# Optimization experiments

Measured on AMD Instinct MI355X. Metric: run time of the kernel, lower is better.

Reference implementation:

```python
import jax, jax.numpy as jnp
import numpy as np

D_MODEL = 1024
H = 16
D_K = D_MODEL // H
D_FF = 4096
EPS = 1e-6
NEG = -1e9


def layer_norm(x, alpha, beta):
    # Custom LN: scalar alpha/beta, unbiased std, eps added to std (not var)
    mean = jnp.mean(x, axis=-1, keepdims=True)
    std = jnp.std(x, axis=-1, ddof=1, keepdims=True)
    return alpha * (x - mean) / (std + EPS) + beta


def setup_inputs() -> dict:
    key = jax.random.key(0)
    ks = jax.random.split(key, 16)
    B, S = 4, 2048
    s = 1.0 / np.sqrt(D_MODEL)
    inp = {
        "x": jax.random.normal(ks[0], (B, S, D_MODEL), dtype=jnp.float32),
        "src_mask": jax.random.randint(ks[1], (B, 1, 1, S), 0, 2, dtype=jnp.int32),
        "wq": jax.random.normal(ks[2], (D_MODEL, D_MODEL), jnp.float32) * s,
        "bq": jnp.zeros((D_MODEL,), jnp.float32),
        "wk": jax.random.normal(ks[3], (D_MODEL, D_MODEL), jnp.float32) * s,
        "bk": jnp.zeros((D_MODEL,), jnp.float32),
        "wv": jax.random.normal(ks[4], (D_MODEL, D_MODEL), jnp.float32) * s,
        "bv": jnp.zeros((D_MODEL,), jnp.float32),
        "wo": jax.random.normal(ks[5], (D_MODEL, D_MODEL), jnp.float32) * s,
        "bo": jnp.zeros((D_MODEL,), jnp.float32),
        "w1": jax.random.normal(ks[6], (D_MODEL, D_FF), jnp.float32) * s,
        "b1": jnp.zeros((D_FF,), jnp.float32),
        "w2": jax.random.normal(ks[7], (D_FF, D_MODEL), jnp.float32) * (1.0 / np.sqrt(D_FF)),
        "b2": jnp.zeros((D_MODEL,), jnp.float32),
        "a1": jnp.ones((1,), jnp.float32),
        "be1": jnp.zeros((1,), jnp.float32),
        "a2": jnp.ones((1,), jnp.float32),
        "be2": jnp.zeros((1,), jnp.float32),
    }
    return inp


def reference(x, src_mask, wq, bq, wk, bk, wv, bv, wo, bo, w1, b1, w2, b2, a1, be1, a2, be2):
    B, S, _ = x.shape

    # --- residual 1: self-attention on pre-LN input (dropout = identity, eval) ---
    xn = layer_norm(x, a1, be1)
    q = (xn @ wq + bq).reshape(B, S, H, D_K).transpose(0, 2, 1, 3)  # [B,H,S,Dk]
    k = (xn @ wk + bk).reshape(B, S, H, D_K).transpose(0, 2, 1, 3)
    v = (xn @ wv + bv).reshape(B, S, H, D_K).transpose(0, 2, 1, 3)

    scores = jnp.einsum("bhqd,bhkd->bhqk", q, k) / jnp.sqrt(jnp.float32(D_K))
    scores = jnp.where(src_mask == 0, jnp.float32(NEG), scores)
    attn = jax.nn.softmax(scores, axis=-1)
    ctx = jnp.einsum("bhqk,bhkd->bhqd", attn, v)  # [B,H,S,Dk]
    ctx = ctx.transpose(0, 2, 1, 3).reshape(B, S, D_MODEL)
    attn_out = ctx @ wo + bo
    x = x + attn_out

    # --- residual 2: feed-forward on pre-LN input ---
    xn2 = layer_norm(x, a2, be2)
    ff = jax.nn.relu(xn2 @ w1 + b1) @ w2 + b2
    return x + ff
```

## Files before the change

kernel.cpp:

```cpp
#include <hip/hip_runtime.h>
#include <stdint.h>

typedef unsigned short u16;
typedef __attribute__((ext_vector_type(8))) short short8;
typedef __attribute__((ext_vector_type(4))) float f32x4;
typedef __attribute__((ext_vector_type(4))) u16 u16x4;
typedef __attribute__((ext_vector_type(4))) uint32_t u32x4;

#define NB 4
#define SEQ 2048
#define DM 1024
#define NH 16
#define DKh 64
#define DFF 4096
#define LOG2E 1.44269504089f

__device__ __forceinline__ u16 f2bf(float f) {
  union { float f; uint32_t u; } v; v.f = f;
  uint32_t u = v.u;
  return (u16)((u + 0x7FFFu + ((u >> 16) & 1u)) >> 16);
}

__device__ __forceinline__ uint32_t cvtpk(float lo, float hi) {
  uint32_t r;
  asm("v_cvt_pk_bf16_f32 %0, %1, %2" : "=v"(r) : "v"(lo), "v"(hi));
  return r;
}

__device__ __forceinline__ float fexp2(float x) {
  float r;
  asm("v_exp_f32 %0, %1" : "=v"(r) : "v"(x));
  return r;
}

__device__ __forceinline__ void gl16(const u16* g, u16* l) {
  __builtin_amdgcn_global_load_lds((const __attribute__((address_space(1))) void*)g,
                                   (__attribute__((address_space(3))) void*)l, 16, 0, 0);
}

__global__ __launch_bounds__(256) void transpose_bf16(const float* __restrict__ src,
                                                      u16* __restrict__ dst, int R, int C) {
  __shared__ float tile[32][33];
  int tx = threadIdx.x, ty = threadIdx.y;
  int c0 = blockIdx.x * 32, r0 = blockIdx.y * 32;
#pragma unroll
  for (int i = 0; i < 32; i += 8)
    tile[ty + i][tx] = src[(size_t)(r0 + ty + i) * C + c0 + tx];
  __syncthreads();
#pragma unroll
  for (int i = 0; i < 32; i += 8)
    dst[(size_t)(c0 + ty + i) * R + r0 + tx] = f2bf(tile[tx][ty + i]);
}

__global__ __launch_bounds__(256) void bias_cat(const float* __restrict__ bq,
                                                const float* __restrict__ bk,
                                                const float* __restrict__ bv,
                                                float* __restrict__ o) {
  int i = blockIdx.x * 256 + threadIdx.x;
  if (i < 3072) o[i] = (i < 1024) ? bq[i] : ((i < 2048) ? bk[i - 1024] : bv[i - 2048]);
}

__global__ __launch_bounds__(1024) void compact_idx(const int* __restrict__ msk,
                                                    int* __restrict__ cidx,
                                                    int* __restrict__ lArr,
                                                    int* __restrict__ lpArr,
                                                    float* __restrict__ fbbc) {
  int b = blockIdx.x;
  int t = threadIdx.x;
  int lane = t & 63, w = t >> 6;
  int i0 = t * 2, i1 = t * 2 + 1;
  int m0 = msk[b * SEQ + i0] ? 1 : 0;
  int m1 = msk[b * SEQ + i1] ? 1 : 0;
  int s = m0 + m1;
  int run = s;
#pragma unroll
  for (int d = 1; d < 64; d <<= 1) {
    int v = __shfl_up(run, d);
    if (lane >= d) run += v;
  }
  __shared__ int wtot[16];
  __shared__ int woff[17];
  if (lane == 63) wtot[w] = run;
  __syncthreads();
  if (t == 0) {
    int acc = 0;
#pragma unroll
    for (int i = 0; i < 16; ++i) { woff[i] = acc; acc += wtot[i]; }
    woff[16] = acc;
  }
  __syncthreads();
  int excl = run - s + woff[w];
  if (m0) cidx[b * SEQ + excl] = i0;
  if (m1) cidx[b * SEQ + excl + m0] = i1;
  int L = woff[16];
  int LP = (L + 63) & ~63;
  if (LP == 0) LP = 64;
  if (t == 0) { lArr[b] = L; lpArr[b] = LP; }
  for (int l = t; l < SEQ; l += 1024) {
    if (l >= L) cidx[b * SEQ + l] = 0;
    fbbc[b * SEQ + l] = (l < L) ? 0.0f : -1e9f;
  }
}

__global__ __launch_bounds__(256) void gather_vt(const u16* __restrict__ vtb,
                                                 const int* __restrict__ cidx,
                                                 const int* __restrict__ lpArr,
                                                 u16* __restrict__ vthat) {
  int d = blockIdx.x;
  int bh = blockIdx.y;
  int b = bh >> 4;
  int t = threadIdx.x;
  __shared__ u16 row[SEQ];
  const u16* src = vtb + ((size_t)bh * DKh + d) * SEQ;
  *(short8*)&row[t * 8] = *(const short8*)(src + t * 8);
  __syncthreads();
  int LP = lpArr[b];
  u16* dst = vthat + ((size_t)bh * DKh + d) * SEQ;
  const int* ib = cidx + b * SEQ;
  for (int l2 = t; l2 * 2 < LP; l2 += 256) {
    uint32_t lo = row[ib[l2 * 2]];
    uint32_t hi = row[ib[l2 * 2 + 1]];
    *(uint32_t*)&dst[l2 * 2] = lo | (hi << 16);
  }
}

__global__ __launch_bounds__(256) void ln_bf16(const float* __restrict__ x,
                                               u16* __restrict__ out,
                                               const float* __restrict__ alpha,
                                               const float* __restrict__ beta) {
  int row = blockIdx.x;
  const float4* xr = (const float4*)(x + (size_t)row * DM);
  int t = threadIdx.x;
  float4 v = xr[t];
  float s = v.x + v.y + v.z + v.w;
  float s2 = v.x * v.x + v.y * v.y + v.z * v.z + v.w * v.w;
#pragma unroll
  for (int m = 1; m < 64; m <<= 1) { s += __shfl_xor(s, m); s2 += __shfl_xor(s2, m); }
  __shared__ float red[8];
  int wid = t >> 6, lane = t & 63;
  if (lane == 0) { red[wid] = s; red[wid + 4] = s2; }
  __syncthreads();
  float S = red[0] + red[1] + red[2] + red[3];
  float S2 = red[4] + red[5] + red[6] + red[7];
  float mean = S * (1.0f / DM);
  float var = fmaxf((S2 - S * mean) * (1.0f / (DM - 1)), 0.0f);
  float inv = alpha[0] / (sqrtf(var) + 1e-6f);
  float bet = beta[0];
  u16x4 o;
  o[0] = f2bf((v.x - mean) * inv + bet);
  o[1] = f2bf((v.y - mean) * inv + bet);
  o[2] = f2bf((v.z - mean) * inv + bet);
  o[3] = f2bf((v.w - mean) * inv + bet);
  *(u16x4*)(out + (size_t)row * DM + t * 4) = o;
}

template <int MODE>
__global__ __launch_bounds__(512, 1) void gemm256(const u16* __restrict__ A,
                                                  const u16* __restrict__ WT,
                                                  const float* __restrict__ bias,
                                                  u16* __restrict__ outp,
                                                  int M, int N, int K, float qscale) {
  extern __shared__ u16 lds[];
  int tid = threadIdx.x;
  int lane = tid & 63, wid = tid >> 6;
  int lr = lane & 15, lg = lane >> 4;
  int wr = wid >> 2, wc = wid & 3;
  int nbx = N >> 8;
  int nwg = (M >> 8) * nbx;
  int lid = blockIdx.x;
  int swz = (lid & 7) * (nwg >> 3) + (lid >> 3);
  int m0 = (swz / nbx) << 8, n0 = (swz % nbx) << 8;

  int rowih = wid * 16 + (lane >> 2);
  int cchunk = lane & 3;
  int csrc = cchunk ^ ((rowih >> 1) & 3);
  size_t a_src = (size_t)(m0 + rowih) * K + csrc * 8;
  size_t b_src = (size_t)(n0 + rowih) * K + csrc * 8;
  u16* a_dst = lds + rowih * 32 + cchunk * 8;
  u16* b_dst = a_dst + 8192;

#define STAGE_A(B_, T_) do { \
    const u16* s_ = A + a_src + (size_t)(T_) * 32; \
    gl16(s_, a_dst + (B_) * 16384); \
    gl16(s_ + (size_t)128 * K, a_dst + (B_) * 16384 + 4096); \
  } while (0)
#define STAGE_B(B_, T_) do { \
    const u16* s_ = WT + b_src + (size_t)(T_) * 32; \
    gl16(s_, b_dst + (B_) * 16384); \
    gl16(s_ + (size_t)128 * K, b_dst + (B_) * 16384 + 4096); \
  } while (0)

  int rchunk = (lg ^ ((lr >> 1) & 3)) * 8;
  int offA[8], offB[4];
#pragma unroll
  for (int i = 0; i < 8; ++i) offA[i] = (wr * 128 + i * 16 + lr) * 32 + rchunk;
#pragma unroll
  for (int j = 0; j < 4; ++j) offB[j] = (wc * 64 + j * 16 + lr) * 32 + rchunk;

  f32x4 acc[8][4] = {};

  int NT = K >> 5;
  STAGE_A(0, 0); STAGE_B(0, 0);
  STAGE_A(1, 1); STAGE_B(1, 1);
  asm volatile("s_waitcnt vmcnt(4)" ::: "memory");
  __builtin_amdgcn_s_barrier();

  int buf = 0;
  for (int t = 0; t < NT; ++t) {
    const u16* la = lds + buf * 16384;
    const u16* lb = la + 8192;
    int b2 = buf - 1; if (b2 < 0) b2 += 3;
    short8 af0[4], bfr[4];
#pragma unroll
    for (int i = 0; i < 4; ++i) af0[i] = *(const short8*)&la[offA[i]];
#pragma unroll
    for (int j = 0; j < 4; ++j) bfr[j] = *(const short8*)&lb[offB[j]];
    if (t + 2 < NT) STAGE_A(b2, t + 2);
    __builtin_amdgcn_s_setprio(1);
#pragma unroll
    for (int i = 0; i < 4; ++i)
#pragma unroll
      for (int j = 0; j < 4; ++j)
        acc[i][j] = __builtin_amdgcn_mfma_f32_16x16x32_bf16(af0[i], bfr[j], acc[i][j], 0, 0, 0);
    __builtin_amdgcn_s_setprio(0);
    short8 af1[4];
#pragma unroll
    for (int i = 0; i < 4; ++i) af1[i] = *(const short8*)&la[offA[i + 4]];
    if (t + 2 < NT) STAGE_B(b2, t + 2);
    if (t < NT - 2) asm volatile("s_waitcnt vmcnt(4)" ::: "memory");
    else            asm volatile("s_waitcnt vmcnt(0)" ::: "memory");
    __builtin_amdgcn_s_setprio(1);
#pragma unroll
    for (int i = 0; i < 4; ++i)
#pragma unroll
      for (int j = 0; j < 4; ++j)
        acc[i + 4][j] = __builtin_amdgcn_mfma_f32_16x16x32_bf16(af1[i], bfr[j], acc[i + 4][j], 0, 0, 0);
    __builtin_amdgcn_s_setprio(0);
    __builtin_amdgcn_s_barrier();
    __builtin_amdgcn_sched_barrier(0);
    buf = (buf == 2) ? 0 : buf + 1;
  }
#undef STAGE_A
#undef STAGE_B

#pragma unroll
  for (int i = 0; i < 8; ++i) {
#pragma unroll
    for (int j = 0; j < 4; ++j) {
      int col = n0 + wc * 64 + j * 16 + lr;
      float bi = bias[col];
      int rbase = m0 + wr * 128 + i * 16 + lg * 4;
      if (MODE == 0) {
        int which = col >> 10, nc = col & 1023;
        int hh = nc >> 6, dd = nc & 63;
        int bb = rbase >> 11, ss = rbase & 2047;
        if (which == 2) {
          u16* vtb = outp + (size_t)2 * (8u << 20);
          u16x4 pk;
#pragma unroll
          for (int r = 0; r < 4; ++r) pk[r] = f2bf(acc[i][j][r] + bi);
          *(u16x4*)&vtb[((size_t)(bb * NH + hh) * DKh + dd) * SEQ + ss] = pk;
        } else {
          u16* dst = outp + (size_t)which * (8u << 20);
          float sc = (which == 0) ? qscale : 1.0f;
#pragma unroll
          for (int r = 0; r < 4; ++r)
            dst[((size_t)(bb * NH + hh) * SEQ + (ss + r)) * DKh + dd] = f2bf((acc[i][j][r] + bi) * sc);
        }
      } else {
#pragma unroll
        for (int r = 0; r < 4; ++r)
          outp[(size_t)(rbase + r) * N + col] = f2bf(fmaxf(acc[i][j][r] + bi, 0.0f));
      }
    }
  }
}

__global__ __launch_bounds__(512, 4) void gemm_v2(const u16* __restrict__ A,
                                                  const u16* __restrict__ WT,
                                                  const float* __restrict__ bias,
                                                  const float* __restrict__ resid,
                                                  float* __restrict__ outp,
                                                  int M, int N, int K) {
  extern __shared__ u16 lds[];
  int tid = threadIdx.x;
  int lane = tid & 63, wid = tid >> 6;
  int lr = lane & 15, lg = lane >> 4;
  int wr = wid >> 1, wc = wid & 1;
  int nbx = N >> 7;
  int nwg = (M >> 8) * nbx;
  int lid = blockIdx.x;
  int swz = (lid & 7) * (nwg >> 3) + (lid >> 3);
  int m0 = (swz / nbx) << 8, n0 = (swz % nbx) << 7;

  int sr = tid >> 2;
  int sch = tid & 3;
  int scs = sch ^ ((sr >> 1) & 3);
  size_t a_src = (size_t)(m0 + sr) * K + scs * 8;
  size_t b_src = (size_t)(n0 + sr) * K + scs * 8;
  u16* a_dst = lds + sr * 32 + sch * 8;
  u16* b_dst = lds + 8192 + sr * 32 + sch * 8;

#define STAGE(B_, T_) do { \
    gl16(A + a_src + (size_t)(T_) * 32, a_dst + (B_) * 12288); \
    gl16(A + a_src + (size_t)128 * K + (size_t)(T_) * 32, a_dst + (B_) * 12288 + 4096); \
    gl16(WT + b_src + (size_t)(T_) * 32, b_dst + (B_) * 12288); \
  } while (0)

  int rchunk = (lg ^ ((lr >> 1) & 3)) * 8;
  int offA[4], offB[4];
#pragma unroll
  for (int i = 0; i < 4; ++i) offA[i] = (wr * 64 + i * 16 + lr) * 32 + rchunk;
#pragma unroll
  for (int j = 0; j < 4; ++j) offB[j] = 8192 + (wc * 64 + j * 16 + lr) * 32 + rchunk;

  f32x4 acc[4][4] = {};

  int NT = K >> 5;
  STAGE(0, 0);
  STAGE(1, 1);
  asm volatile("s_waitcnt vmcnt(3)" ::: "memory");
  __builtin_amdgcn_s_barrier();

  int buf = 0;
  for (int t = 0; t < NT; ++t) {
    const u16* la = lds + buf * 12288;
    int b2 = buf - 1; if (b2 < 0) b2 += 3;
    short8 af[4], bfr[4];
#pragma unroll
    for (int i = 0; i < 4; ++i) af[i] = *(const short8*)&la[offA[i]];
#pragma unroll
    for (int j = 0; j < 4; ++j) bfr[j] = *(const short8*)&la[offB[j]];
    if (t + 2 < NT) STAGE(b2, t + 2);
    __builtin_amdgcn_s_setprio(1);
#pragma unroll
    for (int i = 0; i < 4; ++i)
#pragma unroll
      for (int j = 0; j < 4; ++j)
        acc[i][j] = __builtin_amdgcn_mfma_f32_16x16x32_bf16(af[i], bfr[j], acc[i][j], 0, 0, 0);
    __builtin_amdgcn_s_setprio(0);
    if (t < NT - 2) asm volatile("s_waitcnt vmcnt(3)" ::: "memory");
    else            asm volatile("s_waitcnt vmcnt(0)" ::: "memory");
    __builtin_amdgcn_s_barrier();
    __builtin_amdgcn_sched_barrier(0);
    buf = (buf == 2) ? 0 : buf + 1;
  }
#undef STAGE

#pragma unroll
  for (int i = 0; i < 4; ++i) {
#pragma unroll
    for (int j = 0; j < 4; ++j) {
      int col = n0 + wc * 64 + j * 16 + lr;
      float bi = bias[col];
      int rbase = m0 + wr * 64 + i * 16 + lg * 4;
#pragma unroll
      for (int r = 0; r < 4; ++r) {
        size_t idx = (size_t)(rbase + r) * N + col;
        outp[idx] = resid[idx] + acc[i][j][r] + bi;
      }
    }
  }
}

__global__ __launch_bounds__(256) void attn_fwd(const u16* __restrict__ q,
                                                const u16* __restrict__ k,
                                                const u16* __restrict__ vt,
                                                const int* __restrict__ cidx,
                                                const int* __restrict__ lArr,
                                                const int* __restrict__ lpArr,
                                                const float* __restrict__ fbbc,
                                                u16* __restrict__ ctx) {
  __shared__ u16 Ks[64 * 64];
  __shared__ u16 Vs[64 * 64];
  int tid = threadIdx.x;
  int wid = tid >> 6, lane = tid & 63;
  int lr = lane & 15, lg = lane >> 4;
  int bh = blockIdx.y;
  int b = bh >> 4, hh = bh & 15;
  int q0 = blockIdx.x * 128;
  const u16* qbase = q + (size_t)bh * SEQ * DKh;
  const u16* kbase = k + (size_t)bh * SEQ * DKh;
  const u16* vbase = vt + (size_t)bh * DKh * SEQ;
  const float* fbbase = fbbc + b * SEQ;
  const int* ib = cidx + b * SEQ;
  int Lb = lArr[b];
  int LP = lpArr[b];

  short8 qf[2][2];
#pragma unroll
  for (int i = 0; i < 2; ++i)
#pragma unroll
    for (int kk = 0; kk < 2; ++kk)
      qf[i][kk] = *(const short8*)(qbase + (size_t)(q0 + wid * 32 + i * 16 + lr) * DKh + kk * 32 + lg * 8);

  int sr = tid >> 3;
  int scg = (tid & 7) * 8;
  int kwix[2];
#pragma unroll
  for (int it = 0; it < 2; ++it) {
    int r = it * 32 + sr;
    kwix[it] = r * 64 + (scg ^ ((r & 7) << 3));
  }
  int jsrc = scg >> 4;
  int pos1 = (jsrc & 1) * 32 + ((scg & 15) >> 2) * 8 + (jsrc >> 1) * 4;
  int vwix[2][2];
#pragma unroll
  for (int it = 0; it < 2; ++it) {
    int r = it * 32 + sr;
    int sw = (r & 7) << 3;
    vwix[it][0] = r * 64 + (pos1 ^ sw);
    vwix[it][1] = r * 64 + ((pos1 + 8) ^ sw);
  }
  int swzc = (lr & 7) << 3;

  short8 ka[2], va[2];
  {
    int id0 = ib[sr], id1 = ib[32 + sr];
    ka[0] = *(const short8*)(kbase + (size_t)id0 * DKh + scg);
    ka[1] = *(const short8*)(kbase + (size_t)id1 * DKh + scg);
    va[0] = *(const short8*)(vbase + (size_t)sr * SEQ + scg);
    va[1] = *(const short8*)(vbase + (size_t)(32 + sr) * SEQ + scg);
  }

  f32x4 ot[2][4] = {};
  float mrow[2] = {-3e38f, -3e38f};
  float lsum[2] = {0.0f, 0.0f};

  for (int kv0 = 0; kv0 < LP; kv0 += 64) {
    __syncthreads();
#pragma unroll
    for (int it = 0; it < 2; ++it) {
      *(short8*)&Ks[kwix[it]] = ka[it];
      u16x4 vlo, vhi;
#pragma unroll
      for (int e = 0; e < 4; ++e) { vlo[e] = ((u16*)&va[it])[e]; vhi[e] = ((u16*)&va[it])[e + 4]; }
      *(u16x4*)&Vs[vwix[it][0]] = vlo;
      *(u16x4*)&Vs[vwix[it][1]] = vhi;
    }
    if (kv0 + 64 < LP) {
      int nv = kv0 + 64;
      int id0 = ib[nv + sr], id1 = ib[nv + 32 + sr];
      ka[0] = *(const short8*)(kbase + (size_t)id0 * DKh + scg);
      ka[1] = *(const short8*)(kbase + (size_t)id1 * DKh + scg);
      va[0] = *(const short8*)(vbase + (size_t)sr * SEQ + nv + scg);
      va[1] = *(const short8*)(vbase + (size_t)(32 + sr) * SEQ + nv + scg);
    }
    __syncthreads();

    f32x4 st[2][4] = {};
    __builtin_amdgcn_s_setprio(1);
#pragma unroll
    for (int kk = 0; kk < 2; ++kk) {
      short8 kf[4];
#pragma unroll
      for (int j = 0; j < 4; ++j)
        kf[j] = *(const short8*)&Ks[(j * 16 + lr) * 64 + ((kk * 32 + lg * 8) ^ swzc)];
#pragma unroll
      for (int i = 0; i < 2; ++i)
#pragma unroll
        for (int j = 0; j < 4; ++j)
          st[i][j] = __builtin_amdgcn_mfma_f32_16x16x32_bf16(kf[j], qf[i][kk], st[i][j], 0, 0, 0);
    }
    __builtin_amdgcn_s_setprio(0);

    bool tail = (kv0 + 64 > Lb);

    u32x4 pa[2][2];
#pragma unroll
    for (int i = 0; i < 2; ++i) {
      float p[4][4];
      if (tail) {
#pragma unroll
        for (int j = 0; j < 4; ++j) {
          float4 f4 = *(const float4*)(fbbase + kv0 + j * 16 + lg * 4);
          p[j][0] = st[i][j][0] + f4.x;
          p[j][1] = st[i][j][1] + f4.y;
          p[j][2] = st[i][j][2] + f4.z;
          p[j][3] = st[i][j][3] + f4.w;
        }
      } else {
#pragma unroll
        for (int j = 0; j < 4; ++j)
#pragma unroll
          for (int r = 0; r < 4; ++r) p[j][r] = st[i][j][r];
      }
      float mx = -3e38f;
#pragma unroll
      for (int j = 0; j < 4; ++j)
#pragma unroll
        for (int r = 0; r < 4; ++r) mx = fmaxf(mx, p[j][r]);
      mx = fmaxf(mx, __shfl_xor(mx, 16));
      mx = fmaxf(mx, __shfl_xor(mx, 32));
      float mnew = fmaxf(mrow[i], mx);
      if (!__all(mnew - mrow[i] <= 8.0f)) {
        float corr = fexp2(mrow[i] - mnew);
        lsum[i] *= corr;
#pragma unroll
        for (int jd = 0; jd < 4; ++jd)
#pragma unroll
          for (int r = 0; r < 4; ++r) ot[i][jd][r] *= corr;
        mrow[i] = mnew;
      }
      float ps = 0.0f;
#pragma unroll
      for (int j = 0; j < 4; ++j)
#pragma unroll
        for (int r = 0; r < 4; ++r) {
          float pv = fexp2(p[j][r] - mrow[i]);
          p[j][r] = pv;
          ps += pv;
        }
      ps += __shfl_xor(ps, 16);
      ps += __shfl_xor(ps, 32);
      lsum[i] += ps;
#pragma unroll
      for (int ks = 0; ks < 2; ++ks) {
        pa[i][ks][0] = cvtpk(p[ks][0], p[ks][1]);
        pa[i][ks][1] = cvtpk(p[ks][2], p[ks][3]);
        pa[i][ks][2] = cvtpk(p[ks + 2][0], p[ks + 2][1]);
        pa[i][ks][3] = cvtpk(p[ks + 2][2], p[ks + 2][3]);
      }
    }

    __builtin_amdgcn_s_setprio(1);
#pragma unroll
    for (int ks = 0; ks < 2; ++ks) {
      short8 vf[4];
#pragma unroll
      for (int jd = 0; jd < 4; ++jd)
        vf[jd] = *(const short8*)&Vs[(jd * 16 + lr) * 64 + ((ks * 32 + lg * 8) ^ swzc)];
#pragma unroll
      for (int i = 0; i < 2; ++i)
#pragma unroll
        for (int jd = 0; jd < 4; ++jd)
          ot[i][jd] = __builtin_amdgcn_mfma_f32_16x16x32_bf16(vf[jd], *(short8*)&pa[i][ks], ot[i][jd], 0, 0, 0);
    }
    __builtin_amdgcn_s_setprio(0);
  }

  float inv0 = 1.0f / lsum[0], inv1 = 1.0f / lsum[1];
  __syncthreads();
  u16* ep = (wid < 2) ? (Ks + wid * 2048) : (Vs + (wid - 2) * 2048);
#pragma unroll
  for (int i = 0; i < 2; ++i) {
    float inv = i ? inv1 : inv0;
#pragma unroll
    for (int jd = 0; jd < 4; ++jd) {
      uint32_t w0 = cvtpk(ot[i][jd][0] * inv, ot[i][jd][1] * inv);
      uint32_t w1 = cvtpk(ot[i][jd][2] * inv, ot[i][jd][3] * inv);
      uint32_t pk2[2] = {w0, w1};
      *(u16x4*)&ep[(i * 16 + lr) * 64 + ((jd * 16 + lg * 4) ^ swzc)] = *(u16x4*)pk2;
    }
  }
  __syncthreads();
  int q_ = lane >> 1;
  size_t orow = ((size_t)b * SEQ + q0 + wid * 32 + q_) * DM + hh * DKh;
#pragma unroll
  for (int it = 0; it < 4; ++it) {
    int dc = (lane & 1) * 32 + it * 8;
    short8 vv = *(const short8*)&ep[q_ * 64 + (dc ^ ((q_ & 7) << 3))];
    *(short8*)(ctx + orow + dc) = vv;
  }
}

extern "C" void kernel_launch(void* const* d_in, const int* in_sizes, int n_in,
                              void* d_out, int out_size, void* d_ws, size_t ws_size,
                              hipStream_t stream) {
  const float* x   = (const float*)d_in[0];
  const int*   msk = (const int*)d_in[1];
  const float* wq  = (const float*)d_in[2];
  const float* bq  = (const float*)d_in[3];
  const float* wk  = (const float*)d_in[4];
  const float* bk  = (const float*)d_in[5];
  const float* wv  = (const float*)d_in[6];
  const float* bv  = (const float*)d_in[7];
  const float* wo  = (const float*)d_in[8];
  const float* bo  = (const float*)d_in[9];
  const float* w1  = (const float*)d_in[10];
  const float* b1  = (const float*)d_in[11];
  const float* w2  = (const float*)d_in[12];
  const float* b2  = (const float*)d_in[13];
  const float* a1  = (const float*)d_in[14];
  const float* be1 = (const float*)d_in[15];
  const float* a2  = (const float*)d_in[16];
  const float* be2 = (const float*)d_in[17];
  float* out = (float*)d_out;

  u16* wqT = (u16*)d_ws;
  u16* wkT = wqT + (1u << 20);
  u16* wvT = wkT + (1u << 20);
  u16* woT = wvT + (1u << 20);
  u16* w1T = woT + (1u << 20);
  u16* w2T = w1T + (4u << 20);
  u16* xn  = w2T + (4u << 20);
  u16* qb  = xn  + (8u << 20);
  u16* kb  = qb  + (8u << 20);
  u16* vtb = kb  + (8u << 20);
  u16* ctx = vtb + (8u << 20);
  u16* hb  = qb;
  float* bcat = (float*)ctx;
  int*   cidx = (int*)(ctx + (8u << 20));
  int*   lArr = cidx + NB * SEQ;
  int*   lpArr = lArr + 16;
  float* fbbc = (float*)(lpArr + 16);

  (void)hipFuncSetAttribute((const void*)gemm256<0>, hipFuncAttributeMaxDynamicSharedMemorySize, 96 * 1024);
  (void)hipFuncSetAttribute((const void*)gemm256<3>, hipFuncAttributeMaxDynamicSharedMemorySize, 96 * 1024);
  (void)hipFuncSetAttribute((const void*)gemm_v2, hipFuncAttributeMaxDynamicSharedMemorySize, 72 * 1024);

  dim3 tb(32, 8);
  transpose_bf16<<<dim3(32, 32), tb, 0, stream>>>(wq, wqT, DM, DM);
  transpose_bf16<<<dim3(32, 32), tb, 0, stream>>>(wk, wkT, DM, DM);
  transpose_bf16<<<dim3(32, 32), tb, 0, stream>>>(wv, wvT, DM, DM);
  transpose_bf16<<<dim3(32, 32), tb, 0, stream>>>(wo, woT, DM, DM);
  transpose_bf16<<<dim3(128, 32), tb, 0, stream>>>(w1, w1T, DM, DFF);
  transpose_bf16<<<dim3(32, 128), tb, 0, stream>>>(w2, w2T, DFF, DM);
  bias_cat<<<12, 256, 0, stream>>>(bq, bk, bv, bcat);
  compact_idx<<<NB, 1024, 0, stream>>>(msk, cidx, lArr, lpArr, fbbc);

  ln_bf16<<<NB * SEQ, 256, 0, stream>>>(x, xn, a1, be1);

  gemm256<0><<<384, 512, 96 * 1024, stream>>>(xn, wqT, bcat, qb, NB * SEQ, 3 * DM, DM, 0.125f * LOG2E);

  gather_vt<<<dim3(DKh, NB * NH), 256, 0, stream>>>(vtb, cidx, lpArr, xn);

  attn_fwd<<<dim3(SEQ / 128, NB * NH), 256, 0, stream>>>(qb, kb, xn, cidx, lArr, lpArr, fbbc, ctx);

  gemm_v2<<<256, 512, 72 * 1024, stream>>>(ctx, woT, bo, x, out, NB * SEQ, DM, DM);

  ln_bf16<<<NB * SEQ, 256, 0, stream>>>(out, xn, a2, be2);

  gemm256<3><<<512, 512, 96 * 1024, stream>>>(xn, w1T, b1, hb, NB * SEQ, DFF, DM, 1.0f);

  gemm_v2<<<256, 512, 72 * 1024, stream>>>(hb, w2T, b2, out, out, NB * SEQ, DM, DFF);
}
```

Measured before the change: 376.3 us.

## Scatter compacted K/V in QKV epilogue and async-stage attention tiles

The QKV GEMM epilogue now writes K and V straight into mask-compacted positions using an inverse index map, with V pre-permuted into the layout attention reads. This removes the gather_vt kernel and the indexed K loads inside attention. Attention now double-buffers K/V tiles in LDS through direct global-to-LDS loads, and its grid order changes to head-major. The four square weight transposes are merged into one launch. The cost is scattered 2-byte stores in the GEMM epilogue and more LDS use in attention.

Measured after the change: 376.6 us. Within noise of the previous version (+0.1%).

```diff
diff --git a/kernel.cpp b/kernel.cpp
--- a/kernel.cpp
+++ b/kernel.cpp
@@ -38,6 +38,29 @@
                                    (__attribute__((address_space(3))) void*)l, 16, 0, 0);
 }
 
+__global__ __launch_bounds__(256) void transpose4_bf16(const float* __restrict__ s0,
+                                                       const float* __restrict__ s1,
+                                                       const float* __restrict__ s2,
+                                                       const float* __restrict__ s3,
+                                                       u16* __restrict__ d0,
+                                                       u16* __restrict__ d1,
+                                                       u16* __restrict__ d2,
+                                                       u16* __restrict__ d3) {
+  __shared__ float tile[32][33];
+  int z = blockIdx.z;
+  const float* src = (z == 0) ? s0 : (z == 1) ? s1 : (z == 2) ? s2 : s3;
+  u16* dst = (z == 0) ? d0 : (z == 1) ? d1 : (z == 2) ? d2 : d3;
+  int tx = threadIdx.x, ty = threadIdx.y;
+  int c0 = blockIdx.x * 32, r0 = blockIdx.y * 32;
+#pragma unroll
+  for (int i = 0; i < 32; i += 8)
+    tile[ty + i][tx] = src[(size_t)(r0 + ty + i) * DM + c0 + tx];
+  __syncthreads();
+#pragma unroll
+  for (int i = 0; i < 32; i += 8)
+    dst[(size_t)(c0 + ty + i) * DM + r0 + tx] = f2bf(tile[tx][ty + i]);
+}
+
 __global__ __launch_bounds__(256) void transpose_bf16(const float* __restrict__ src,
                                                       u16* __restrict__ dst, int R, int C) {
   __shared__ float tile[32][33];
@@ -61,7 +84,7 @@
 }
 
 __global__ __launch_bounds__(1024) void compact_idx(const int* __restrict__ msk,
-                                                    int* __restrict__ cidx,
+                                                    int* __restrict__ pinv,
                                                     int* __restrict__ lArr,
                                                     int* __restrict__ lpArr,
                                                     float* __restrict__ fbbc) {
@@ -90,38 +113,17 @@
   }
   __syncthreads();
   int excl = run - s + woff[w];
-  if (m0) cidx[b * SEQ + excl] = i0;
-  if (m1) cidx[b * SEQ + excl + m0] = i1;
+  pinv[b * SEQ + i0] = m0 ? excl : -1;
+  pinv[b * SEQ + i1] = m1 ? (excl + m0) : -1;
   int L = woff[16];
-  int LP = (L + 63) & ~63;
-  if (LP == 0) LP = 64;
-  if (t == 0) { lArr[b] = L; lpArr[b] = LP; }
-  for (int l = t; l < SEQ; l += 1024) {
-    if (l >= L) cidx[b * SEQ + l] = 0;
+  if (t == 0) {
+    lArr[b] = L;
+    int LP = (L + 63) & ~63;
+    if (LP == 0) LP = 64;
+    lpArr[b] = LP;
+  }
+  for (int l = t; l < SEQ; l += 1024)
     fbbc[b * SEQ + l] = (l < L) ? 0.0f : -1e9f;
-  }
-}
-
-__global__ __launch_bounds__(256) void gather_vt(const u16* __restrict__ vtb,
-                                                 const int* __restrict__ cidx,
-                                                 const int* __restrict__ lpArr,
-                                                 u16* __restrict__ vthat) {
-  int d = blockIdx.x;
-  int bh = blockIdx.y;
-  int b = bh >> 4;
-  int t = threadIdx.x;
-  __shared__ u16 row[SEQ];
-  const u16* src = vtb + ((size_t)bh * DKh + d) * SEQ;
-  *(short8*)&row[t * 8] = *(const short8*)(src + t * 8);
-  __syncthreads();
-  int LP = lpArr[b];
-  u16* dst = vthat + ((size_t)bh * DKh + d) * SEQ;
-  const int* ib = cidx + b * SEQ;
-  for (int l2 = t; l2 * 2 < LP; l2 += 256) {
-    uint32_t lo = row[ib[l2 * 2]];
-    uint32_t hi = row[ib[l2 * 2 + 1]];
-    *(uint32_t*)&dst[l2 * 2] = lo | (hi << 16);
-  }
 }
 
 __global__ __launch_bounds__(256) void ln_bf16(const float* __restrict__ x,
@@ -159,6 +161,7 @@
                                                   const u16* __restrict__ WT,
                                                   const float* __restrict__ bias,
                                                   u16* __restrict__ outp,
+                                                  const int* __restrict__ pinv,
                                                   int M, int N, int K, float qscale) {
   extern __shared__ u16 lds[];
   int tid = threadIdx.x;
@@ -254,18 +257,31 @@
         int which = col >> 10, nc = col & 1023;
         int hh = nc >> 6, dd = nc & 63;
         int bb = rbase >> 11, ss = rbase & 2047;
-        if (which == 2) {
-          u16* vtb = outp + (size_t)2 * (8u << 20);
-          u16x4 pk;
-#pragma unroll
-          for (int r = 0; r < 4; ++r) pk[r] = f2bf(acc[i][j][r] + bi);
-          *(u16x4*)&vtb[((size_t)(bb * NH + hh) * DKh + dd) * SEQ + ss] = pk;
+        if (which == 0) {
+          u16* dst = outp;
+#pragma unroll
+          for (int r = 0; r < 4; ++r)
+            dst[((size_t)(bb * NH + hh) * SEQ + (ss + r)) * DKh + dd] = f2bf((acc[i][j][r] + bi) * qscale);
         } else {
-          u16* dst = outp + (size_t)which * (8u << 20);
-          float sc = (which == 0) ? qscale : 1.0f;
-#pragma unroll
-          for (int r = 0; r < 4; ++r)
-            dst[((size_t)(bb * NH + hh) * SEQ + (ss + r)) * DKh + dd] = f2bf((acc[i][j][r] + bi) * sc);
+          int4 p4 = *(const int4*)(pinv + bb * SEQ + ss);
+          int pos[4] = {p4.x, p4.y, p4.z, p4.w};
+          if (which == 1) {
+            u16* kcb = outp + (size_t)(8u << 20);
+#pragma unroll
+            for (int r = 0; r < 4; ++r)
+              if (pos[r] >= 0)
+                kcb[((size_t)(bb * NH + hh) * SEQ + pos[r]) * DKh + dd] = f2bf(acc[i][j][r] + bi);
+          } else {
+            u16* vcb = outp + (size_t)2 * (8u << 20);
+#pragma unroll
+            for (int r = 0; r < 4; ++r)
+              if (pos[r] >= 0) {
+                int l = pos[r];
+                int lo = l & 63;
+                int pi = ((lo >> 4) & 1) * 32 + ((lo >> 2) & 3) * 8 + (lo >> 5) * 4 + (lo & 3);
+                vcb[((size_t)(bb * NH + hh) * DKh + dd) * SEQ + (l & ~63) + pi] = f2bf(acc[i][j][r] + bi);
+              }
+          }
         }
       } else {
 #pragma unroll
@@ -364,26 +380,23 @@
 }
 
 __global__ __launch_bounds__(256) void attn_fwd(const u16* __restrict__ q,
-                                                const u16* __restrict__ k,
-                                                const u16* __restrict__ vt,
-                                                const int* __restrict__ cidx,
+                                                const u16* __restrict__ kc,
+                                                const u16* __restrict__ vc,
                                                 const int* __restrict__ lArr,
                                                 const int* __restrict__ lpArr,
                                                 const float* __restrict__ fbbc,
                                                 u16* __restrict__ ctx) {
-  __shared__ u16 Ks[64 * 64];
-  __shared__ u16 Vs[64 * 64];
+  __shared__ u16 lds[2][8192];
   int tid = threadIdx.x;
   int wid = tid >> 6, lane = tid & 63;
   int lr = lane & 15, lg = lane >> 4;
-  int bh = blockIdx.y;
+  int bh = blockIdx.x;
   int b = bh >> 4, hh = bh & 15;
-  int q0 = blockIdx.x * 128;
+  int q0 = blockIdx.y * 128;
   const u16* qbase = q + (size_t)bh * SEQ * DKh;
-  const u16* kbase = k + (size_t)bh * SEQ * DKh;
-  const u16* vbase = vt + (size_t)bh * DKh * SEQ;
+  const u16* kcb = kc + (size_t)bh * SEQ * DKh;
+  const u16* vcb = vc + (size_t)bh * DKh * SEQ;
   const float* fbbase = fbbc + b * SEQ;
-  const int* ib = cidx + b * SEQ;
   int Lb = lArr[b];
   int LP = lpArr[b];
 
@@ -394,59 +407,33 @@
     for (int kk = 0; kk < 2; ++kk)
       qf[i][kk] = *(const short8*)(qbase + (size_t)(q0 + wid * 32 + i * 16 + lr) * DKh + kk * 32 + lg * 8);
 
-  int sr = tid >> 3;
-  int scg = (tid & 7) * 8;
-  int kwix[2];
-#pragma unroll
-  for (int it = 0; it < 2; ++it) {
-    int r = it * 32 + sr;
-    kwix[it] = r * 64 + (scg ^ ((r & 7) << 3));
-  }
-  int jsrc = scg >> 4;
-  int pos1 = (jsrc & 1) * 32 + ((scg & 15) >> 2) * 8 + (jsrc >> 1) * 4;
-  int vwix[2][2];
-#pragma unroll
-  for (int it = 0; it < 2; ++it) {
-    int r = it * 32 + sr;
-    int sw = (r & 7) << 3;
-    vwix[it][0] = r * 64 + (pos1 ^ sw);
-    vwix[it][1] = r * 64 + ((pos1 + 8) ^ sw);
-  }
+  int srow = tid >> 3;
+  int schk = tid & 7;
+  int ks0 = srow * 64 + ((schk ^ (srow & 7)) * 8);
+  int vs0 = srow * SEQ + ((schk ^ (srow & 7)) * 8);
+  int dst0 = tid * 8;
+
+#define STAGE(B_, KV0) do { \
+    gl16(kcb + (size_t)(KV0) * 64 + ks0, &lds[B_][dst0]); \
+    gl16(kcb + (size_t)(KV0) * 64 + ks0 + 2048, &lds[B_][dst0 + 2048]); \
+    gl16(vcb + (size_t)(KV0) + vs0, &lds[B_][dst0 + 4096]); \
+    gl16(vcb + (size_t)(KV0) + vs0 + 32 * SEQ, &lds[B_][dst0 + 6144]); \
+  } while (0)
+
   int swzc = (lr & 7) << 3;
-
-  short8 ka[2], va[2];
-  {
-    int id0 = ib[sr], id1 = ib[32 + sr];
-    ka[0] = *(const short8*)(kbase + (size_t)id0 * DKh + scg);
-    ka[1] = *(const short8*)(kbase + (size_t)id1 * DKh + scg);
-    va[0] = *(const short8*)(vbase + (size_t)sr * SEQ + scg);
-    va[1] = *(const short8*)(vbase + (size_t)(32 + sr) * SEQ + scg);
-  }
 
   f32x4 ot[2][4] = {};
   float mrow[2] = {-3e38f, -3e38f};
   float lsum[2] = {0.0f, 0.0f};
 
+  STAGE(0, 0);
+  __syncthreads();
+
+  int buf = 0;
   for (int kv0 = 0; kv0 < LP; kv0 += 64) {
-    __syncthreads();
-#pragma unroll
-    for (int it = 0; it < 2; ++it) {
-      *(short8*)&Ks[kwix[it]] = ka[it];
-      u16x4 vlo, vhi;
-#pragma unroll
-      for (int e = 0; e < 4; ++e) { vlo[e] = ((u16*)&va[it])[e]; vhi[e] = ((u16*)&va[it])[e + 4]; }
-      *(u16x4*)&Vs[vwix[it][0]] = vlo;
-      *(u16x4*)&Vs[vwix[it][1]] = vhi;
-    }
-    if (kv0 + 64 < LP) {
-      int nv = kv0 + 64;
-      int id0 = ib[nv + sr], id1 = ib[nv + 32 + sr];
-      ka[0] = *(const short8*)(kbase + (size_t)id0 * DKh + scg);
-      ka[1] = *(const short8*)(kbase + (size_t)id1 * DKh + scg);
-      va[0] = *(const short8*)(vbase + (size_t)sr * SEQ + nv + scg);
-      va[1] = *(const short8*)(vbase + (size_t)(32 + sr) * SEQ + nv + scg);
-    }
-    __syncthreads();
+    if (kv0 + 64 < LP) STAGE(buf ^ 1, kv0 + 64);
+    const u16* Ks = lds[buf];
+    const u16* Vs = lds[buf] + 4096;
 
     f32x4 st[2][4] = {};
     __builtin_amdgcn_s_setprio(1);
@@ -537,11 +524,13 @@
           ot[i][jd] = __builtin_amdgcn_mfma_f32_16x16x32_bf16(vf[jd], *(short8*)&pa[i][ks], ot[i][jd], 0, 0, 0);
     }
     __builtin_amdgcn_s_setprio(0);
-  }
+    __syncthreads();
+    buf ^= 1;
+  }
+#undef STAGE
 
   float inv0 = 1.0f / lsum[0], inv1 = 1.0f / lsum[1];
-  __syncthreads();
-  u16* ep = (wid < 2) ? (Ks + wid * 2048) : (Vs + (wid - 2) * 2048);
+  u16* ep = &lds[0][wid * 2048];
 #pragma unroll
   for (int i = 0; i < 2; ++i) {
     float inv = i ? inv1 : inv0;
@@ -600,8 +589,8 @@
   u16* ctx = vtb + (8u << 20);
   u16* hb  = qb;
   float* bcat = (float*)ctx;
-  int*   cidx = (int*)(ctx + (8u << 20));
-  int*   lArr = cidx + NB * SEQ;
+  int*   pinv = (int*)(ctx + (8u << 20));
+  int*   lArr = pinv + NB * SEQ;
   int*   lpArr = lArr + 16;
   float* fbbc = (float*)(lpArr + 16);
 
@@ -610,28 +599,23 @@
   (void)hipFuncSetAttribute((const void*)gemm_v2, hipFuncAttributeMaxDynamicSharedMemorySize, 72 * 1024);
 
   dim3 tb(32, 8);
-  transpose_bf16<<<dim3(32, 32), tb, 0, stream>>>(wq, wqT, DM, DM);
-  transpose_bf16<<<dim3(32, 32), tb, 0, stream>>>(wk, wkT, DM, DM);
-  transpose_bf16<<<dim3(32, 32), tb, 0, stream>>>(wv, wvT, DM, DM);
-  transpose_bf16<<<dim3(32, 32), tb, 0, stream>>>(wo, woT, DM, DM);
+  transpose4_bf16<<<dim3(32, 32, 4), tb, 0, stream>>>(wq, wk, wv, wo, wqT, wkT, wvT, woT);
   transpose_bf16<<<dim3(128, 32), tb, 0, stream>>>(w1, w1T, DM, DFF);
   transpose_bf16<<<dim3(32, 128), tb, 0, stream>>>(w2, w2T, DFF, DM);
   bias_cat<<<12, 256, 0, stream>>>(bq, bk, bv, bcat);
-  compact_idx<<<NB, 1024, 0, stream>>>(msk, cidx, lArr, lpArr, fbbc);
+  compact_idx<<<NB, 1024, 0, stream>>>(msk, pinv, lArr, lpArr, fbbc);
 
   ln_bf16<<<NB * SEQ, 256, 0, stream>>>(x, xn, a1, be1);
 
-  gemm256<0><<<384, 512, 96 * 1024, stream>>>(xn, wqT, bcat, qb, NB * SEQ, 3 * DM, DM, 0.125f * LOG2E);
-
-  gather_vt<<<dim3(DKh, NB * NH), 256, 0, stream>>>(vtb, cidx, lpArr, xn);
-
-  attn_fwd<<<dim3(SEQ / 128, NB * NH), 256, 0, stream>>>(qb, kb, xn, cidx, lArr, lpArr, fbbc, ctx);
+  gemm256<0><<<384, 512, 96 * 1024, stream>>>(xn, wqT, bcat, qb, pinv, NB * SEQ, 3 * DM, DM, 0.125f * LOG2E);
+
+  attn_fwd<<<dim3(NB * NH, SEQ / 128), 256, 0, stream>>>(qb, kb, vtb, lArr, lpArr, fbbc, ctx);
 
   gemm_v2<<<256, 512, 72 * 1024, stream>>>(ctx, woT, bo, x, out, NB * SEQ, DM, DM);
 
   ln_bf16<<<NB * SEQ, 256, 0, stream>>>(out, xn, a2, be2);
 
-  gemm256<3><<<512, 512, 96 * 1024, stream>>>(xn, w1T, b1, hb, NB * SEQ, DFF, DM, 1.0f);
+  gemm256<3><<<512, 512, 96 * 1024, stream>>>(xn, w1T, b1, hb, nullptr, NB * SEQ, DFF, DM, 1.0f);
 
   gemm_v2<<<256, 512, 72 * 1024, stream>>>(hb, w2T, b2, out, out, NB * SEQ, DM, DFF);
 }
```
